# Kernel optimization log

Measured on AMD Instinct MI355X. Metric: run time of the kernel, lower is better.

## Reference

```python
import jax, jax.numpy as jnp
import numpy as np

N = 50000      # nodes
E = 800000     # edges
HID = 64       # hidden_dim
HEADS = 4
DH = HID // HEADS
PIN = 128      # person_in_dim
DIN = 64       # disease_in_dim
NEXP = 4       # num_experts
K = 2          # topk
L = 2          # n_layers
NEG = 0.2      # gat_neg_slope


def setup_inputs() -> dict:
    key = jax.random.key(0)
    ks = iter(jax.random.split(key, 64))
    nrm = lambda shp, s=0.05: jax.random.normal(next(ks), shp, jnp.float32) * s
    d = {}
    d["features"] = jax.random.normal(next(ks), (N, PIN), jnp.float32)
    d["node_types"] = jax.random.randint(next(ks), (N,), 0, 2)
    d["src"] = jax.random.randint(next(ks), (E,), 0, N)
    d["dst"] = jax.random.randint(next(ks), (E,), 0, N)
    d["W_person"] = nrm((PIN, HID)); d["b_person"] = jnp.zeros((HID,), jnp.float32)
    d["W_disease"] = nrm((DIN, HID)); d["b_disease"] = jnp.zeros((HID,), jnp.float32)
    d["gat_W"] = nrm((L, HID, HID)); d["gat_al"] = nrm((L, HEADS, DH)); d["gat_ar"] = nrm((L, HEADS, DH))
    d["gin_eps"] = jnp.zeros((L,), jnp.float32)
    d["gin_W1"] = nrm((L, HID, HID)); d["gin_b1"] = jnp.zeros((L, HID), jnp.float32)
    d["gin_W2"] = nrm((L, HID, HID)); d["gin_b2"] = jnp.zeros((L, HID), jnp.float32)
    for p in ("gat", "gin"):
        d[p + "_gW"] = nrm((HID, NEXP)); d[p + "_gb"] = jnp.zeros((NEXP,), jnp.float32)
        d[p + "_eW1"] = nrm((NEXP, HID, HID // 2)); d[p + "_eb1"] = jnp.zeros((NEXP, HID // 2), jnp.float32)
        d[p + "_eW2"] = nrm((NEXP, HID // 2, HID)); d[p + "_eb2"] = jnp.zeros((NEXP, HID), jnp.float32)
    d["fg_W1"] = nrm((2 * HID, HID)); d["fg_b1"] = jnp.zeros((HID,), jnp.float32)
    d["fg_W2"] = nrm((HID, HID)); d["fg_b2"] = jnp.zeros((HID,), jnp.float32)
    return d


def _edge_softmax(logits, dst):
    m = jax.ops.segment_max(logits, dst, num_segments=N)
    e = jnp.exp(logits - m[dst])
    s = jax.ops.segment_sum(e, dst, num_segments=N)
    return e / (s[dst] + 1e-9)


def _gat(h, src, dst, gat_W, gat_al, gat_ar):
    for l in range(L):
        hW = (h @ gat_W[l]).reshape(N, HEADS, DH)
        el = (hW * gat_al[l]).sum(-1)                    # [N, HEADS]
        er = (hW * gat_ar[l]).sum(-1)
        lg = jax.nn.leaky_relu(el[src] + er[dst], NEG)   # [E, HEADS]
        a = _edge_softmax(lg, dst)
        out = jax.ops.segment_sum(hW[src] * a[:, :, None], dst, num_segments=N)
        h2 = out.reshape(N, HID) + h                     # residual=True
        h = jax.nn.relu(h2) if l < L - 1 else h2
    return h


def _gin(h, src, dst, gin_eps, gin_W1, gin_b1, gin_W2, gin_b2):
    deg = jax.ops.segment_sum(jnp.ones((E,), jnp.float32), dst, num_segments=N)
    inv = 1.0 / jnp.maximum(deg, 1.0)
    for l in range(L):
        agg = jax.ops.segment_sum(h[src], dst, num_segments=N) * inv[:, None]  # 'mean' aggregator
        x = (1.0 + gin_eps[l]) * h + agg                 # learn_eps=True
        x = jax.nn.relu(x @ gin_W1[l] + gin_b1[l]) @ gin_W2[l] + gin_b2[l]     # 2-layer MLP
        h = jax.nn.relu(x) if l < L - 1 else x
    return h


def _expert(h, gW, gb, eW1, eb1, eW2, eb2):
    probs = jax.nn.softmax(h @ gW + gb, axis=-1)         # [N, NEXP]
    topv, topi = jax.lax.top_k(probs, K)
    topv = topv / topv.sum(-1, keepdims=True)
    hot = jax.nn.one_hot(topi, NEXP, dtype=h.dtype)      # [N, K, NEXP]
    w = (hot * topv[..., None]).sum(1)                   # [N, NEXP] sparse weights
    e1 = jax.nn.relu(jnp.einsum('nd,edh->neh', h, eW1) + eb1)
    e2 = jnp.einsum('neh,ehd->ned', e1, eW2) + eb2       # [N, NEXP, HID]
    out = (e2 * w[:, :, None]).sum(1)
    f = hot.sum(1).mean(0)                               # routed fraction per expert
    P = probs.mean(0)
    aux = NEXP * jnp.sum(f * P)                          # switch-style load balancing
    return out, aux


def reference(features, node_types, src, dst, W_person, b_person, W_disease, b_disease,
              gat_W, gat_al, gat_ar, gin_eps, gin_W1, gin_b1, gin_W2, gin_b2,
              gat_gW, gat_gb, gat_eW1, gat_eb1, gat_eW2, gat_eb2,
              gin_gW, gin_gb, gin_eW1, gin_eb1, gin_eW2, gin_eb2,
              fg_W1, fg_b1, fg_W2, fg_b2):
    # per-type projection + scatter into shared buffer
    hp = features[:, :PIN] @ W_person + b_person
    hd = features[:, :DIN] @ W_disease + b_disease
    h = jnp.where((node_types == 0)[:, None], hp, hd)
    z_gat = _gat(h, src, dst, gat_W, gat_al, gat_ar)
    z_gin = _gin(h, src, dst, gin_eps, gin_W1, gin_b1, gin_W2, gin_b2)
    zg, aux_g = _expert(z_gat, gat_gW, gat_gb, gat_eW1, gat_eb1, gat_eW2, gat_eb2)
    zi, aux_i = _expert(z_gin, gin_gW, gin_gb, gin_eW1, gin_eb1, gin_eW2, gin_eb2)
    z = zi * zg
    u = jnp.concatenate([zg, zi], axis=-1)
    gate = jax.nn.sigmoid(jax.nn.relu(u @ fg_W1 + fg_b1) @ fg_W2 + fg_b2)
    u_prime = gate  # source calls fusion_gate(u) twice -> identical deterministic value
    z = gate * z + (1.0 - gate) * u_prime
    return z, aux_i + aux_g
```

## Files before the change

### kernel.cpp

```cpp
#include <hip/hip_runtime.h>

#define NN 50000
#define EE 800000
#define NEG 0.2f
#define NBLK_SCAN 196
#define NBG 391
#define NBE 196
#define NBKT 98
#define EPB 4096
#define NSEG 196

typedef __attribute__((ext_vector_type(8))) short s8;
typedef __attribute__((ext_vector_type(4))) float f4;

__device__ __forceinline__ float leaky(float x) { return x > 0.f ? x : NEG * x; }
__device__ __forceinline__ unsigned bf16r(float x) {
    unsigned u = __float_as_uint(x);
    return (u + 0x7fffu + ((u >> 16) & 1u)) >> 16;
}
__device__ __forceinline__ float lo16(unsigned p) { return __uint_as_float(p << 16); }
__device__ __forceinline__ float hi16(unsigned p) { return __uint_as_float(p & 0xffff0000u); }

__device__ __forceinline__ s8 a_from_f32(const float* p) {
    float4 u = *reinterpret_cast<const float4*>(p);
    float4 v = *reinterpret_cast<const float4*>(p + 4);
    s8 r;
    r[0] = (short)bf16r(u.x); r[1] = (short)bf16r(u.y);
    r[2] = (short)bf16r(u.z); r[3] = (short)bf16r(u.w);
    r[4] = (short)bf16r(v.x); r[5] = (short)bf16r(v.y);
    r[6] = (short)bf16r(v.z); r[7] = (short)bf16r(v.w);
    return r;
}

__global__ __launch_bounds__(256) void k_binA(const int* __restrict__ src,
        const int* __restrict__ dst, int* __restrict__ degcnt,
        int* __restrict__ seg_off, int* __restrict__ seg_cnt,
        unsigned* __restrict__ gseg) {
    __shared__ int cnt[NBKT];
    __shared__ int pre[128];
    __shared__ unsigned sbuf[EPB];
    for (int i = threadIdx.x; i < NBKT; i += 256) cnt[i] = 0;
    __syncthreads();
    int e0 = blockIdx.x * EPB;
    int nE = EE - e0; if (nE > EPB) nE = EPB;
    int b[16]; unsigned val[16]; int rk[16];
    #pragma unroll
    for (int i = 0; i < 16; i++) {
        int li = i * 256 + threadIdx.x;
        if (li < nE) {
            int e = e0 + li;
            int d = dst[e], s = src[e];
            atomicAdd(&degcnt[d], 1);
            b[i] = d >> 9;
            val[i] = ((unsigned)s << 9) | (unsigned)(d & 511);
            rk[i] = atomicAdd(&cnt[b[i]], 1);
        } else b[i] = -1;
    }
    __syncthreads();
    if (threadIdx.x < 128) pre[threadIdx.x] = (threadIdx.x < NBKT) ? cnt[threadIdx.x] : 0;
    __syncthreads();
    for (int off = 1; off < 128; off <<= 1) {
        int v = 0;
        if (threadIdx.x < 128 && threadIdx.x >= off) v = pre[threadIdx.x - off];
        __syncthreads();
        if (threadIdx.x < 128) pre[threadIdx.x] += v;
        __syncthreads();
    }
    #pragma unroll
    for (int i = 0; i < 16; i++)
        if (b[i] >= 0) sbuf[pre[b[i]] - cnt[b[i]] + rk[i]] = val[i];
    if (threadIdx.x < NBKT) {
        seg_off[blockIdx.x * NBKT + threadIdx.x] = pre[threadIdx.x] - cnt[threadIdx.x];
        seg_cnt[blockIdx.x * NBKT + threadIdx.x] = cnt[threadIdx.x];
    }
    __syncthreads();
    for (int i = threadIdx.x; i < nE; i += 256)
        gseg[(size_t)blockIdx.x * EPB + i] = sbuf[i];
}

__global__ void k_scan_a(const int* __restrict__ degcnt, int* __restrict__ bsums) {
    __shared__ int sm[4];
    int i = blockIdx.x * 256 + threadIdx.x;
    int v = (i < NN) ? degcnt[i] : 0;
    #pragma unroll
    for (int o = 1; o < 64; o <<= 1) v += __shfl_xor(v, o, 64);
    if ((threadIdx.x & 63) == 0) sm[threadIdx.x >> 6] = v;
    __syncthreads();
    if (threadIdx.x == 0) bsums[blockIdx.x] = sm[0] + sm[1] + sm[2] + sm[3];
}

__global__ void k_scan_b(const int* __restrict__ bsums, int* __restrict__ bpre) {
    __shared__ int sm[256];
    int t = threadIdx.x;
    sm[t] = (t < NBLK_SCAN) ? bsums[t] : 0;
    __syncthreads();
    for (int off = 1; off < 256; off <<= 1) {
        int u = (t >= off) ? sm[t - off] : 0;
        __syncthreads();
        sm[t] += u;
        __syncthreads();
    }
    if (t < NBLK_SCAN) bpre[t] = (t == 0) ? 0 : sm[t - 1];
}

__global__ void k_scan_c(const int* __restrict__ degcnt, const int* __restrict__ bpre,
                         int* __restrict__ row_start) {
    __shared__ int sm[256];
    int t = threadIdx.x;
    int i = blockIdx.x * 256 + t;
    int v = (i < NN) ? degcnt[i] : 0;
    sm[t] = v;
    __syncthreads();
    for (int off = 1; off < 256; off <<= 1) {
        int u = (t >= off) ? sm[t - off] : 0;
        __syncthreads();
        sm[t] += u;
        __syncthreads();
    }
    int incl = sm[t];
    if (i < NN) row_start[i] = bpre[blockIdx.x] + incl - v;
    if (i == NN - 1) row_start[NN] = bpre[blockIdx.x] + incl;
}

__global__ __launch_bounds__(256) void k_binB_pre(
        const int* __restrict__ row_start, const int* __restrict__ seg_off,
        const int* __restrict__ seg_cnt, const unsigned* __restrict__ gseg,
        int* __restrict__ csr_src,
        const float* __restrict__ feat, const int* __restrict__ types,
        const float* __restrict__ Wp, const float* __restrict__ bp,
        const float* __restrict__ Wd, const float* __restrict__ bd,
        const float* __restrict__ gW, const float* __restrict__ al,
        const float* __restrict__ ar,
        float* __restrict__ h0f, unsigned* __restrict__ P,
        float* __restrict__ el, float* __restrict__ er) {
    __shared__ unsigned short WpT[64 * 136];
    __shared__ unsigned short WdT[64 * 72];
    __shared__ unsigned short WgT[64 * 72];
    __shared__ unsigned short y0s[4][16 * 72];
    __shared__ int kur[512];
    if (blockIdx.x < NBKT) {
        int b = blockIdx.x;
        int t = threadIdx.x;
        int* spre = (int*)WpT;
        int* soff = (int*)WdT;
        int* ss   = (int*)WgT;
        int c0 = (2 * t     < NSEG) ? seg_cnt[(2 * t)     * NBKT + b] : 0;
        int c1 = (2 * t + 1 < NSEG) ? seg_cnt[(2 * t + 1) * NBKT + b] : 0;
        if (2 * t     < NSEG) soff[2 * t]     = seg_off[(2 * t)     * NBKT + b];
        if (2 * t + 1 < NSEG) soff[2 * t + 1] = seg_off[(2 * t + 1) * NBKT + b];
        ss[t] = c0 + c1;
        __syncthreads();
        for (int off = 1; off < 256; off <<= 1) {
            int u = (t >= off) ? ss[t - off] : 0;
            __syncthreads();
            ss[t] += u;
            __syncthreads();
        }
        int base = ss[t] - (c0 + c1);
        if (2 * t     < NSEG) spre[2 * t]     = base;
        if (2 * t + 1 < NSEG) spre[2 * t + 1] = base + c0;
        if (t == 0) spre[NSEG] = ss[255];
        int d0 = b << 9;
        for (int i = t; i < 512; i += 256) {
            int d = d0 + i;
            kur[i] = (d < NN) ? row_start[d] : 0;
        }
        __syncthreads();
        int cntb = spre[NSEG];
        for (int idx = t; idx < cntb; idx += 256) {
            int lo = 0, hi = NSEG - 1;
            #pragma unroll
            for (int s = 0; s < 8; s++) {
                int mid = (lo + hi + 1) >> 1;
                if (spre[mid] <= idx) lo = mid; else hi = mid - 1;
            }
            unsigned v = gseg[(size_t)lo * EPB + soff[lo] + (idx - spre[lo])];
            int p = atomicAdd(&kur[v & 511], 1);
            csr_src[p] = (int)(v >> 9);
        }
        return;
    }
    for (int idx = threadIdx.x; idx < 128 * 64; idx += 256) {
        int k = idx >> 6, n = idx & 63;
        WpT[n * 136 + k] = (unsigned short)bf16r(Wp[idx]);
    }
    for (int idx = threadIdx.x; idx < 64 * 64; idx += 256) {
        int k = idx >> 6, n = idx & 63;
        WdT[n * 72 + k] = (unsigned short)bf16r(Wd[idx]);
        WgT[n * 72 + k] = (unsigned short)bf16r(gW[idx]);
    }
    __syncthreads();
    int wv = threadIdx.x >> 6, lane = threadIdx.x & 63;
    int quad = lane >> 4, l16 = lane & 15;
    int gw2 = (blockIdx.x - NBKT) * 4 + wv;
    int mtEnd = gw2 * 2 + 2; if (mtEnd > 3125) mtEnd = 3125;
    for (int mt = gw2 * 2; mt < mtEnd; mt++) {
        int row0 = mt * 16;
        const float* arow = feat + (size_t)(row0 + l16) * 128;
        f4 accp[4], accd[4];
        #pragma unroll
        for (int t = 0; t < 4; t++) { accp[t] = f4{0.f,0.f,0.f,0.f}; accd[t] = f4{0.f,0.f,0.f,0.f}; }
        #pragma unroll
        for (int ks = 0; ks < 4; ks++) {
            s8 a = a_from_f32(arow + ks * 32 + quad * 8);
            #pragma unroll
            for (int t = 0; t < 4; t++) {
                s8 b = *(const s8*)&WpT[(t * 16 + l16) * 136 + ks * 32 + quad * 8];
                accp[t] = __builtin_amdgcn_mfma_f32_16x16x32_bf16(a, b, accp[t], 0, 0, 0);
                if (ks < 2) {
                    s8 bd_ = *(const s8*)&WdT[(t * 16 + l16) * 72 + ks * 32 + quad * 8];
                    accd[t] = __builtin_amdgcn_mfma_f32_16x16x32_bf16(a, bd_, accd[t], 0, 0, 0);
                }
            }
        }
        int ty[4];
        #pragma unroll
        for (int r = 0; r < 4; r++) ty[r] = types[row0 + quad * 4 + r];
        float vv[4][4];
        #pragma unroll
        for (int t = 0; t < 4; t++) {
            int col = t * 16 + l16;
            float bpv = bp[col], bdv = bd[col];
            #pragma unroll
            for (int r = 0; r < 4; r++) {
                float v = ty[r] ? (accd[t][r] + bdv) : (accp[t][r] + bpv);
                vv[t][r] = v;
                h0f[(size_t)(row0 + quad * 4 + r) * 64 + col] = v;
                y0s[wv][(quad * 4 + r) * 72 + col] = (unsigned short)bf16r(v);
            }
        }
        s8 a0 = *(const s8*)&y0s[wv][l16 * 72 + quad * 8];
        s8 a1 = *(const s8*)&y0s[wv][l16 * 72 + 32 + quad * 8];
        f4 hw[4];
        #pragma unroll
        for (int t = 0; t < 4; t++) {
            hw[t] = f4{0.f,0.f,0.f,0.f};
            s8 b0 = *(const s8*)&WgT[(t * 16 + l16) * 72 + quad * 8];
            hw[t] = __builtin_amdgcn_mfma_f32_16x16x32_bf16(a0, b0, hw[t], 0, 0, 0);
            s8 b1_ = *(const s8*)&WgT[(t * 16 + l16) * 72 + 32 + quad * 8];
            hw[t] = __builtin_amdgcn_mfma_f32_16x16x32_bf16(a1, b1_, hw[t], 0, 0, 0);
        }
        #pragma unroll
        for (int t = 0; t < 4; t++) {
            int col = t * 16 + l16;
            float alv = al[col], arv = ar[col];
            #pragma unroll
            for (int r = 0; r < 4; r++) {
                int row = row0 + quad * 4 + r;
                float h = hw[t][r];
                P[(size_t)row * 64 + col] = bf16r(h) | (bf16r(vv[t][r]) << 16);
                float pl = h * alv, pr = h * arv;
                #pragma unroll
                for (int m = 1; m < 16; m <<= 1) {
                    pl += __shfl_xor(pl, m, 64);
                    pr += __shfl_xor(pr, m, 64);
                }
                if (l16 == 0) {
                    el[(size_t)row * 4 + t] = pl;
                    er[(size_t)row * 4 + t] = pr;
                }
            }
        }
    }
}

template <int RELU>
__global__ void k_edges(const int* __restrict__ rows, const int* __restrict__ csr,
                        const unsigned* __restrict__ Pin,
                        const float* __restrict__ el, const float* __restrict__ er,
                        const float* __restrict__ gat_in, const float* __restrict__ gin_in,
                        const float* __restrict__ eps_p,
                        float* __restrict__ vgf, unsigned short* __restrict__ vgb,
                        unsigned short* __restrict__ xb) {
    __shared__ float ews[4][256];
    int wv = threadIdx.x >> 6, lane = threadIdx.x & 63;
    int n = blockIdx.x * 4 + wv;
    int st = rows[n], dg = rows[n + 1] - st;
    int hd = lane >> 4;
    float4 erv = *reinterpret_cast<const float4*>(er + (size_t)n * 4);
    float accg = 0.f, acci = 0.f, ssum = 0.f;
    for (int base = 0; base < dg; base += 64) {
        int rem = dg - base; if (rem > 64) rem = 64;
        int myi = 0;
        if (lane < rem) {
            myi = csr[st + base + lane];
            float4 lv = *reinterpret_cast<const float4*>(el + (size_t)myi * 4);
            float4 ev;
            ev.x = __expf(leaky(lv.x + erv.x));
            ev.y = __expf(leaky(lv.y + erv.y));
            ev.z = __expf(leaky(lv.z + erv.z));
            ev.w = __expf(leaky(lv.w + erv.w));
            *reinterpret_cast<float4*>(&ews[wv][lane * 4]) = ev;
        }
        int j = 0;
        for (; j + 4 <= rem; j += 4) {
            int s0 = __shfl(myi, j, 64),     s1 = __shfl(myi, j + 1, 64);
            int s2 = __shfl(myi, j + 2, 64), s3 = __shfl(myi, j + 3, 64);
            unsigned p0 = Pin[(size_t)s0 * 64 + lane];
            unsigned p1 = Pin[(size_t)s1 * 64 + lane];
            unsigned p2 = Pin[(size_t)s2 * 64 + lane];
            unsigned p3 = Pin[(size_t)s3 * 64 + lane];
            float a0 = ews[wv][(j + 0) * 4 + hd];
            float a1 = ews[wv][(j + 1) * 4 + hd];
            float a2 = ews[wv][(j + 2) * 4 + hd];
            float a3 = ews[wv][(j + 3) * 4 + hd];
            accg += a0 * lo16(p0) + a1 * lo16(p1) + a2 * lo16(p2) + a3 * lo16(p3);
            acci += hi16(p0) + hi16(p1) + hi16(p2) + hi16(p3);
            ssum += a0 + a1 + a2 + a3;
        }
        for (; j < rem; j++) {
            int s0 = __shfl(myi, j, 64);
            unsigned p0 = Pin[(size_t)s0 * 64 + lane];
            float a0 = ews[wv][j * 4 + hd];
            accg += a0 * lo16(p0); acci += hi16(p0); ssum += a0;
        }
    }
    float vg = accg / (ssum + 1e-9f) + gat_in[(size_t)n * 64 + lane];
    if (RELU) vg = fmaxf(vg, 0.f);
    float invd = 1.0f / fmaxf((float)dg, 1.0f);
    float x = (1.0f + eps_p[0]) * gin_in[(size_t)n * 64 + lane] + acci * invd;
    size_t off = (size_t)n * 64 + lane;
    vgf[off] = vg;
    vgb[off] = (unsigned short)bf16r(vg);
    xb[off] = (unsigned short)bf16r(x);
}

template <int L>
__global__ __launch_bounds__(256) void k_mlp(const unsigned short* __restrict__ Gx,
        const unsigned short* __restrict__ Eb,
        const float* __restrict__ W1, const float* __restrict__ b1,
        const float* __restrict__ W2, const float* __restrict__ b2,
        const float* __restrict__ gatW, const float* __restrict__ al,
        const float* __restrict__ ar,
        unsigned short* __restrict__ Fb, float* __restrict__ Cf,
        unsigned* __restrict__ P, float* __restrict__ el, float* __restrict__ er,
        const float* __restrict__ Zg, const float* __restrict__ ggW,
        const float* __restrict__ ggb, const float* __restrict__ igW,
        const float* __restrict__ igb,
        float* __restrict__ wgtg, float* __restrict__ wgti,
        float* __restrict__ stats) {
    __shared__ unsigned short W1T[64 * 72];
    __shared__ unsigned short W2T[64 * 72];
    __shared__ unsigned short WgT[(L == 0) ? 64 * 72 : 64];
    __shared__ unsigned short y1s[4][16 * 72];
    __shared__ float sstat[16];
    if (L == 1 && threadIdx.x < 16) sstat[threadIdx.x] = 0.f;
    for (int idx = threadIdx.x; idx < 64 * 64; idx += 256) {
        int k = idx >> 6, n = idx & 63;
        W1T[n * 72 + k] = (unsigned short)bf16r(W1[idx]);
        W2T[n * 72 + k] = (unsigned short)bf16r(W2[idx]);
        if (L == 0) WgT[n * 72 + k] = (unsigned short)bf16r(gatW[idx]);
    }
    __syncthreads();
    int wv = threadIdx.x >> 6, lane = threadIdx.x & 63;
    int quad = lane >> 4, l16 = lane & 15;
    int gw = blockIdx.x * 4 + wv;
    int mtEnd = gw * 2 + 2; if (mtEnd > 3125) mtEnd = 3125;
    float sp[2][4] = {{0,0,0,0},{0,0,0,0}};
    float sh[2][4] = {{0,0,0,0},{0,0,0,0}};
    for (int mt = gw * 2; mt < mtEnd; mt++) {
        int row0 = mt * 16;
        const unsigned short* arow = Gx + (size_t)(row0 + l16) * 64;
        s8 a0 = *(const s8*)(arow + quad * 8);
        s8 a1 = *(const s8*)(arow + 32 + quad * 8);
        f4 acc1[4];
        #pragma unroll
        for (int t = 0; t < 4; t++) {
            acc1[t] = f4{0.f,0.f,0.f,0.f};
            s8 b0 = *(const s8*)&W1T[(t * 16 + l16) * 72 + quad * 8];
            acc1[t] = __builtin_amdgcn_mfma_f32_16x16x32_bf16(a0, b0, acc1[t], 0, 0, 0);
            s8 b1_ = *(const s8*)&W1T[(t * 16 + l16) * 72 + 32 + quad * 8];
            acc1[t] = __builtin_amdgcn_mfma_f32_16x16x32_bf16(a1, b1_, acc1[t], 0, 0, 0);
        }
        #pragma unroll
        for (int t = 0; t < 4; t++) {
            float b1v = b1[t * 16 + l16];
            #pragma unroll
            for (int r = 0; r < 4; r++) {
                float v = fmaxf(acc1[t][r] + b1v, 0.f);
                y1s[wv][(quad * 4 + r) * 72 + t * 16 + l16] = (unsigned short)bf16r(v);
            }
        }
        s8 c0 = *(const s8*)&y1s[wv][l16 * 72 + quad * 8];
        s8 c1 = *(const s8*)&y1s[wv][l16 * 72 + 32 + quad * 8];
        f4 acc2[4];
        #pragma unroll
        for (int t = 0; t < 4; t++) {
            acc2[t] = f4{0.f,0.f,0.f,0.f};
            s8 b0 = *(const s8*)&W2T[(t * 16 + l16) * 72 + quad * 8];
            acc2[t] = __builtin_amdgcn_mfma_f32_16x16x32_bf16(c0, b0, acc2[t], 0, 0, 0);
            s8 b1_ = *(const s8*)&W2T[(t * 16 + l16) * 72 + 32 + quad * 8];
            acc2[t] = __builtin_amdgcn_mfma_f32_16x16x32_bf16(c1, b1_, acc2[t], 0, 0, 0);
        }
        unsigned short vb[4][4];
        float vout[4][4];
        #pragma unroll
        for (int t = 0; t < 4; t++) {
            int col = t * 16 + l16;
            float b2v = b2[col];
            #pragma unroll
            for (int r = 0; r < 4; r++) {
                float v = acc2[t][r] + b2v;
                if (L == 0) v = fmaxf(v, 0.f);
                size_t off = (size_t)(row0 + quad * 4 + r) * 64 + col;
                unsigned short vb16 = (unsigned short)bf16r(v);
                vb[t][r] = vb16;
                vout[t][r] = v;
                Fb[off] = vb16;
                if (L == 0) Cf[off] = v;
            }
        }
        if (L == 0) {
            const unsigned short* erow = Eb + (size_t)(row0 + l16) * 64;
            s8 e0 = *(const s8*)(erow + quad * 8);
            s8 e1 = *(const s8*)(erow + 32 + quad * 8);
            f4 hw[4];
            #pragma unroll
            for (int t = 0; t < 4; t++) {
                hw[t] = f4{0.f,0.f,0.f,0.f};
                s8 b0 = *(const s8*)&WgT[(t * 16 + l16) * 72 + quad * 8];
                hw[t] = __builtin_amdgcn_mfma_f32_16x16x32_bf16(e0, b0, hw[t], 0, 0, 0);
                s8 b1_ = *(const s8*)&WgT[(t * 16 + l16) * 72 + 32 + quad * 8];
                hw[t] = __builtin_amdgcn_mfma_f32_16x16x32_bf16(e1, b1_, hw[t], 0, 0, 0);
            }
            #pragma unroll
            for (int t = 0; t < 4; t++) {
                int col = t * 16 + l16;
                float alv = al[col], arv = ar[col];
                #pragma unroll
                for (int r = 0; r < 4; r++) {
                    int row = row0 + quad * 4 + r;
                    float h = hw[t][r];
                    P[(size_t)row * 64 + col] = bf16r(h) | ((unsigned)vb[t][r] << 16);
                    float pl = h * alv, pr = h * arv;
                    #pragma unroll
                    for (int m = 1; m < 16; m <<= 1) {
                        pl += __shfl_xor(pl, m, 64);
                        pr += __shfl_xor(pr, m, 64);
                    }
                    if (l16 == 0) {
                        el[(size_t)row * 4 + t] = pl;
                        er[(size_t)row * 4 + t] = pr;
                    }
                }
            }
        } else {
            #pragma unroll
            for (int r = 0; r < 4; r++) {
                int row = row0 + quad * 4 + r;
                float pg[4] = {0,0,0,0}, pi[4] = {0,0,0,0};
                #pragma unroll
                for (int t = 0; t < 4; t++) {
                    int col = t * 16 + l16;
                    float zgv = Zg[(size_t)row * 64 + col];
                    float ziv = vout[t][r];
                    #pragma unroll
                    for (int e = 0; e < 4; e++) {
                        pg[e] += zgv * ggW[col * 4 + e];
                        pi[e] += ziv * igW[col * 4 + e];
                    }
                }
                #pragma unroll
                for (int m = 1; m < 16; m <<= 1) {
                    #pragma unroll
                    for (int e = 0; e < 4; e++) {
                        pg[e] += __shfl_xor(pg[e], m, 64);
                        pi[e] += __shfl_xor(pi[e], m, 64);
                    }
                }
                if (l16 == 0) {
                    #pragma unroll
                    for (int q = 0; q < 2; q++) {
                        float lg0 = (q ? pi[0] + igb[0] : pg[0] + ggb[0]);
                        float lg1 = (q ? pi[1] + igb[1] : pg[1] + ggb[1]);
                        float lg2 = (q ? pi[2] + igb[2] : pg[2] + ggb[2]);
                        float lg3 = (q ? pi[3] + igb[3] : pg[3] + ggb[3]);
                        float mx = fmaxf(fmaxf(lg0, lg1), fmaxf(lg2, lg3));
                        float ex0 = __expf(lg0 - mx), ex1 = __expf(lg1 - mx);
                        float ex2 = __expf(lg2 - mx), ex3 = __expf(lg3 - mx);
                        float inv = 1.0f / (ex0 + ex1 + ex2 + ex3);
                        float pr4[4] = {ex0 * inv, ex1 * inv, ex2 * inv, ex3 * inv};
                        int i1 = 0; float v1 = pr4[0];
                        #pragma unroll
                        for (int t = 1; t < 4; t++) if (pr4[t] > v1) { v1 = pr4[t]; i1 = t; }
                        int i2 = -1; float v2 = -1.f;
                        #pragma unroll
                        for (int t = 0; t < 4; t++) if (t != i1 && pr4[t] > v2) { v2 = pr4[t]; i2 = t; }
                        float wsum = v1 + v2;
                        float wq[4] = {0.f, 0.f, 0.f, 0.f};
                        wq[i1] = v1 / wsum; wq[i2] = v2 / wsum;
                        float* WD = q ? wgti : wgtg;
                        *reinterpret_cast<float4*>(WD + (size_t)row * 4) =
                            float4{wq[0], wq[1], wq[2], wq[3]};
                        #pragma unroll
                        for (int t = 0; t < 4; t++) sp[q][t] += pr4[t];
                        sh[q][i1] += 1.f; sh[q][i2] += 1.f;
                    }
                }
            }
        }
    }
    if (L == 1) {
        __syncthreads();
        if (l16 == 0) {
            #pragma unroll
            for (int q = 0; q < 2; q++)
                #pragma unroll
                for (int e = 0; e < 4; e++) {
                    atomicAdd(&sstat[q * 8 + e], sp[q][e]);
                    atomicAdd(&sstat[q * 8 + 4 + e], sh[q][e]);
                }
        }
        __syncthreads();
        if (threadIdx.x < 16) atomicAdd(&stats[threadIdx.x], sstat[threadIdx.x]);
    }
}

__global__ __launch_bounds__(256) void k_expert(const unsigned short* __restrict__ Eb,
        const unsigned short* __restrict__ Fb,
        const float* __restrict__ g_eW1, const float* __restrict__ g_eb1,
        const float* __restrict__ g_eW2, const float* __restrict__ g_eb2,
        const float* __restrict__ i_eW1, const float* __restrict__ i_eb1,
        const float* __restrict__ i_eW2, const float* __restrict__ i_eb2,
        const float* __restrict__ wgtg, const float* __restrict__ wgti,
        float* __restrict__ moegf, float* __restrict__ moeif,
        unsigned short* __restrict__ ub) {
    __shared__ unsigned short w1t[4 * 32 * 72];
    __shared__ unsigned short w2t[4 * 64 * 40];
    __shared__ unsigned short y1s[4][16 * 40];
    int p = (blockIdx.x >= NBE) ? 1 : 0;
    int bb = blockIdx.x - p * NBE;
    const unsigned short* Ab = p ? Fb : Eb;
    const float* eW1 = p ? i_eW1 : g_eW1;
    const float* eb1 = p ? i_eb1 : g_eb1;
    const float* eW2 = p ? i_eW2 : g_eW2;
    const float* eb2 = p ? i_eb2 : g_eb2;
    const float* wgt = p ? wgti : wgtg;
    float* moef = p ? moeif : moegf;
    int qoff = p ? 64 : 0;
    for (int g = threadIdx.x; g < 8192; g += 256) {
        int e = g >> 11, rem = g & 2047;
        int k = rem >> 5, n = rem & 31;
        w1t[e * 2304 + n * 72 + k] = (unsigned short)bf16r(eW1[g]);
    }
    for (int g = threadIdx.x; g < 8192; g += 256) {
        int e = g >> 11, rem = g & 2047;
        int k = rem >> 6, n = rem & 63;
        w2t[e * 2560 + n * 40 + k] = (unsigned short)bf16r(eW2[g]);
    }
    __syncthreads();
    int wv = threadIdx.x >> 6, lane = threadIdx.x & 63;
    int quad = lane >> 4, l16 = lane & 15;
    int gw = bb * 4 + wv;
    int mtEnd = gw * 4 + 4; if (mtEnd > 3125) mtEnd = 3125;
    for (int mt = gw * 4; mt < mtEnd; mt++) {
        int row0 = mt * 16;
        const unsigned short* arow = Ab + (size_t)(row0 + l16) * 64;
        s8 a0 = *(const s8*)(arow + quad * 8);
        s8 a1 = *(const s8*)(arow + 32 + quad * 8);
        f4 outacc[4];
        #pragma unroll
        for (int t = 0; t < 4; t++) outacc[t] = f4{0.f,0.f,0.f,0.f};
        for (int e = 0; e < 4; e++) {
            f4 acc1[2];
            #pragma unroll
            for (int t = 0; t < 2; t++) {
                acc1[t] = f4{0.f,0.f,0.f,0.f};
                s8 b0 = *(const s8*)&w1t[e * 2304 + (t * 16 + l16) * 72 + quad * 8];
                acc1[t] = __builtin_amdgcn_mfma_f32_16x16x32_bf16(a0, b0, acc1[t], 0, 0, 0);
                s8 b1_ = *(const s8*)&w1t[e * 2304 + (t * 16 + l16) * 72 + 32 + quad * 8];
                acc1[t] = __builtin_amdgcn_mfma_f32_16x16x32_bf16(a1, b1_, acc1[t], 0, 0, 0);
            }
            #pragma unroll
            for (int t = 0; t < 2; t++) {
                float b1v = eb1[e * 32 + t * 16 + l16];
                #pragma unroll
                for (int r = 0; r < 4; r++) {
                    float v = fmaxf(acc1[t][r] + b1v, 0.f);
                    y1s[wv][(quad * 4 + r) * 40 + t * 16 + l16] = (unsigned short)bf16r(v);
                }
            }
            s8 a2 = *(const s8*)&y1s[wv][l16 * 40 + quad * 8];
            f4 acc2[4];
            #pragma unroll
            for (int t = 0; t < 4; t++) {
                acc2[t] = f4{0.f,0.f,0.f,0.f};
                s8 b2_ = *(const s8*)&w2t[e * 2560 + (t * 16 + l16) * 40 + quad * 8];
                acc2[t] = __builtin_amdgcn_mfma_f32_16x16x32_bf16(a2, b2_, acc2[t], 0, 0, 0);
            }
            #pragma unroll
            for (int t = 0; t < 4; t++) {
                float b2v = eb2[e * 64 + t * 16 + l16];
                #pragma unroll
                for (int r = 0; r < 4; r++) {
                    float we = wgt[(size_t)(row0 + quad * 4 + r) * 4 + e];
                    outacc[t][r] += we * (acc2[t][r] + b2v);
                }
            }
        }
        #pragma unroll
        for (int t = 0; t < 4; t++) {
            int col = t * 16 + l16;
            #pragma unroll
            for (int r = 0; r < 4; r++) {
                int row = row0 + quad * 4 + r;
                float v = outacc[t][r];
                moef[(size_t)row * 64 + col] = v;
                ub[(size_t)row * 128 + qoff + col] = (unsigned short)bf16r(v);
            }
        }
    }
}

__global__ __launch_bounds__(256) void k_fusion(const unsigned short* __restrict__ ubuf,
        const float* __restrict__ W1, const float* __restrict__ b1,
        const float* __restrict__ W2, const float* __restrict__ b2,
        const float* __restrict__ moegf, const float* __restrict__ moeif,
        float* __restrict__ out, const float* __restrict__ stats) {
    __shared__ unsigned short W1T[64 * 136];
    __shared__ unsigned short W2T[64 * 72];
    __shared__ unsigned short y1s[4][16 * 72];
    for (int idx = threadIdx.x; idx < 128 * 64; idx += 256) {
        int k = idx >> 6, n = idx & 63;
        W1T[n * 136 + k] = (unsigned short)bf16r(W1[idx]);
    }
    for (int idx = threadIdx.x; idx < 64 * 64; idx += 256) {
        int k = idx >> 6, n = idx & 63;
        W2T[n * 72 + k] = (unsigned short)bf16r(W2[idx]);
    }
    __syncthreads();
    int wv = threadIdx.x >> 6, lane = threadIdx.x & 63;
    int quad = lane >> 4, l16 = lane & 15;
    int gw = blockIdx.x * 4 + wv;
    int mtEnd = gw * 2 + 2; if (mtEnd > 3125) mtEnd = 3125;
    for (int mt = gw * 2; mt < mtEnd; mt++) {
        int row0 = mt * 16;
        const unsigned short* arow = ubuf + (size_t)(row0 + l16) * 128;
        f4 acc1[4];
        #pragma unroll
        for (int t = 0; t < 4; t++) acc1[t] = f4{0.f,0.f,0.f,0.f};
        #pragma unroll
        for (int ks = 0; ks < 4; ks++) {
            s8 a = *(const s8*)(arow + ks * 32 + quad * 8);
            #pragma unroll
            for (int t = 0; t < 4; t++) {
                s8 b = *(const s8*)&W1T[(t * 16 + l16) * 136 + ks * 32 + quad * 8];
                acc1[t] = __builtin_amdgcn_mfma_f32_16x16x32_bf16(a, b, acc1[t], 0, 0, 0);
            }
        }
        #pragma unroll
        for (int t = 0; t < 4; t++) {
            float b1v = b1[t * 16 + l16];
            #pragma unroll
            for (int r = 0; r < 4; r++) {
                float v = fmaxf(acc1[t][r] + b1v, 0.f);
                y1s[wv][(quad * 4 + r) * 72 + t * 16 + l16] = (unsigned short)bf16r(v);
            }
        }
        f4 acc2[4];
        #pragma unroll
        for (int t = 0; t < 4; t++) acc2[t] = f4{0.f,0.f,0.f,0.f};
        #pragma unroll
        for (int ks = 0; ks < 2; ks++) {
            s8 a = *(const s8*)&y1s[wv][l16 * 72 + ks * 32 + quad * 8];
            #pragma unroll
            for (int t = 0; t < 4; t++) {
                s8 b = *(const s8*)&W2T[(t * 16 + l16) * 72 + ks * 32 + quad * 8];
                acc2[t] = __builtin_amdgcn_mfma_f32_16x16x32_bf16(a, b, acc2[t], 0, 0, 0);
            }
        }
        #pragma unroll
        for (int t = 0; t < 4; t++) {
            int col = t * 16 + l16;
            float b2v = b2[col];
            #pragma unroll
            for (int r = 0; r < 4; r++) {
                int row = row0 + quad * 4 + r;
                float g = 1.0f / (1.0f + __expf(-(acc2[t][r] + b2v)));
                float zgv = moegf[(size_t)row * 64 + col];
                float ziv = moeif[(size_t)row * 64 + col];
                out[(size_t)row * 64 + col] = g * zgv * ziv + (1.0f - g) * g;
            }
        }
    }
    if (blockIdx.x == 0 && threadIdx.x < 64) {
        int t = threadIdx.x;
        float s = (t < 16) ? stats[t] : 0.f;
        float aux = 0.f;
        for (int q = 0; q < 2; q++) {
            float a = 0.f;
            for (int e = 0; e < 4; e++) {
                float pr = __shfl(s, q * 8 + e, 64);
                float f  = __shfl(s, q * 8 + 4 + e, 64);
                a += (f / (float)NN) * (pr / (float)NN);
            }
            aux += 4.0f * a;
        }
        if (t == 0) out[(size_t)NN * 64] = aux;
    }
}

extern "C" void kernel_launch(void* const* d_in, const int* in_sizes, int n_in,
                              void* d_out, int out_size, void* d_ws, size_t ws_size,
                              hipStream_t stream) {
    (void)in_sizes; (void)n_in; (void)out_size; (void)ws_size;
    const float* features  = (const float*)d_in[0];
    const int*   node_types= (const int*)d_in[1];
    const int*   src       = (const int*)d_in[2];
    const int*   dst       = (const int*)d_in[3];
    const float* W_person  = (const float*)d_in[4];
    const float* b_person  = (const float*)d_in[5];
    const float* W_disease = (const float*)d_in[6];
    const float* b_disease = (const float*)d_in[7];
    const float* gat_W     = (const float*)d_in[8];
    const float* gat_al    = (const float*)d_in[9];
    const float* gat_ar    = (const float*)d_in[10];
    const float* gin_eps   = (const float*)d_in[11];
    const float* gin_W1    = (const float*)d_in[12];
    const float* gin_b1    = (const float*)d_in[13];
    const float* gin_W2    = (const float*)d_in[14];
    const float* gin_b2    = (const float*)d_in[15];
    const float* gat_gW    = (const float*)d_in[16];
    const float* gat_gb    = (const float*)d_in[17];
    const float* gat_eW1   = (const float*)d_in[18];
    const float* gat_eb1   = (const float*)d_in[19];
    const float* gat_eW2   = (const float*)d_in[20];
    const float* gat_eb2   = (const float*)d_in[21];
    const float* gin_gW    = (const float*)d_in[22];
    const float* gin_gb    = (const float*)d_in[23];
    const float* gin_eW1   = (const float*)d_in[24];
    const float* gin_eb1   = (const float*)d_in[25];
    const float* gin_eW2   = (const float*)d_in[26];
    const float* gin_eb2   = (const float*)d_in[27];
    const float* fg_W1     = (const float*)d_in[28];
    const float* fg_b1     = (const float*)d_in[29];
    const float* fg_W2     = (const float*)d_in[30];
    const float* fg_b2     = (const float*)d_in[31];
    float* out = (float*)d_out;

    float* ws = (float*)d_ws;
    size_t o = 0;
    float* A = ws + o; o += (size_t)NN * 64;
    float* B = ws + o; o += (size_t)NN * 64;
    float* C = ws + o; o += (size_t)NN * 64;
    unsigned short* E  = (unsigned short*)(ws + o); o += (size_t)NN * 32;
    unsigned short* F  = (unsigned short*)(ws + o); o += (size_t)NN * 32;
    unsigned short* G  = (unsigned short*)(ws + o); o += (size_t)NN * 32;
    unsigned* P = (unsigned*)(ws + o); o += (size_t)NN * 64;
    float* el = ws + o; o += (size_t)NN * 4;
    float* er = ws + o; o += (size_t)NN * 4;
    float* wgtg = ws + o; o += (size_t)NN * 4;
    float* wgti = ws + o; o += (size_t)NN * 4;
    int* degcnt    = (int*)(ws + o); o += NN;
    float* stats   = ws + o; o += 16;
    int* row_start = (int*)(ws + o); o += NN + 4;
    int* bsums     = (int*)(ws + o); o += 256;
    int* bpre      = (int*)(ws + o); o += 256;
    int* csr_src   = (int*)(ws + o); o += EE;
    int* seg_off   = (int*)(ws + o); o += NSEG * NBKT + 64;
    int* seg_cnt   = (int*)(ws + o); o += NSEG * NBKT + 64;
    unsigned* gseg = (unsigned*)(ws + o); o += (size_t)NSEG * EPB;

    unsigned short* ub = (unsigned short*)A;

    const int NB_node = NN / 4;

    hipMemsetAsync(degcnt, 0, sizeof(int) * NN + sizeof(float) * 16, stream);

    k_binA<<<NSEG, 256, 0, stream>>>(src, dst, degcnt, seg_off, seg_cnt, gseg);
    k_scan_a<<<NBLK_SCAN, 256, 0, stream>>>(degcnt, bsums);
    k_scan_b<<<1, 256, 0, stream>>>(bsums, bpre);
    k_scan_c<<<NBLK_SCAN, 256, 0, stream>>>(degcnt, bpre, row_start);

    k_binB_pre<<<NBKT + NBG, 256, 0, stream>>>(row_start, seg_off, seg_cnt, gseg, csr_src,
                                               features, node_types, W_person, b_person,
                                               W_disease, b_disease, gat_W, gat_al, gat_ar,
                                               A, P, el, er);

    k_edges<1><<<NB_node, 256, 0, stream>>>(row_start, csr_src, P, el, er, A, A,
                                            gin_eps, B, E, G);
    k_mlp<0><<<NBG, 256, 0, stream>>>(G, E, gin_W1, gin_b1, gin_W2, gin_b2,
                                      gat_W + 4096, gat_al + 64, gat_ar + 64,
                                      F, C, P, el, er,
                                      nullptr, nullptr, nullptr, nullptr, nullptr,
                                      nullptr, nullptr, nullptr);

    k_edges<0><<<NB_node, 256, 0, stream>>>(row_start, csr_src, P, el, er, B, C,
                                            gin_eps + 1, B, E, G);
    k_mlp<1><<<NBG, 256, 0, stream>>>(G, nullptr, gin_W1 + 4096, gin_b1 + 64,
                                      gin_W2 + 4096, gin_b2 + 64,
                                      nullptr, nullptr, nullptr,
                                      F, nullptr, nullptr, nullptr, nullptr,
                                      B, gat_gW, gat_gb, gin_gW, gin_gb,
                                      wgtg, wgti, stats);

    k_expert<<<NBE * 2, 256, 0, stream>>>(E, F,
                                          gat_eW1, gat_eb1, gat_eW2, gat_eb2,
                                          gin_eW1, gin_eb1, gin_eW2, gin_eb2,
                                          wgtg, wgti, B, C, ub);

    k_fusion<<<NBG, 256, 0, stream>>>(ub, fg_W1, fg_b1, fg_W2, fg_b2, B, C, out, stats);
}
```

Before: 351.5 us.

## Derive CSR row offsets inside bucket pass, drop global degree atomics and scans

Removes the per-edge global atomic degree count and the three-kernel prefix scan that built row_start. Instead, k_binA accumulates per-bucket totals, and each bucket block in k_binB_pre counts its own destination degrees in shared memory, scans them locally and writes row_start itself. This saves 800k global atomics, three launches and the large memset. The cost is that each bucket block now reads its gseg entries twice, once to count and once to scatter.

```diff
diff --git a/kernel.cpp b/kernel.cpp
--- a/kernel.cpp
+++ b/kernel.cpp
@@ -3,7 +3,6 @@
 #define NN 50000
 #define EE 800000
 #define NEG 0.2f
-#define NBLK_SCAN 196
 #define NBG 391
 #define NBE 196
 #define NBKT 98
@@ -33,9 +32,9 @@
 }
 
 __global__ __launch_bounds__(256) void k_binA(const int* __restrict__ src,
-        const int* __restrict__ dst, int* __restrict__ degcnt,
+        const int* __restrict__ dst,
         int* __restrict__ seg_off, int* __restrict__ seg_cnt,
-        unsigned* __restrict__ gseg) {
+        unsigned* __restrict__ gseg, int* __restrict__ bucket_tot) {
     __shared__ int cnt[NBKT];
     __shared__ int pre[128];
     __shared__ unsigned sbuf[EPB];
@@ -50,7 +49,6 @@
         if (li < nE) {
             int e = e0 + li;
             int d = dst[e], s = src[e];
-            atomicAdd(&degcnt[d], 1);
             b[i] = d >> 9;
             val[i] = ((unsigned)s << 9) | (unsigned)(d & 511);
             rk[i] = atomicAdd(&cnt[b[i]], 1);
@@ -72,60 +70,17 @@
     if (threadIdx.x < NBKT) {
         seg_off[blockIdx.x * NBKT + threadIdx.x] = pre[threadIdx.x] - cnt[threadIdx.x];
         seg_cnt[blockIdx.x * NBKT + threadIdx.x] = cnt[threadIdx.x];
+        atomicAdd(&bucket_tot[threadIdx.x], cnt[threadIdx.x]);
     }
     __syncthreads();
     for (int i = threadIdx.x; i < nE; i += 256)
         gseg[(size_t)blockIdx.x * EPB + i] = sbuf[i];
 }
 
-__global__ void k_scan_a(const int* __restrict__ degcnt, int* __restrict__ bsums) {
-    __shared__ int sm[4];
-    int i = blockIdx.x * 256 + threadIdx.x;
-    int v = (i < NN) ? degcnt[i] : 0;
-    #pragma unroll
-    for (int o = 1; o < 64; o <<= 1) v += __shfl_xor(v, o, 64);
-    if ((threadIdx.x & 63) == 0) sm[threadIdx.x >> 6] = v;
-    __syncthreads();
-    if (threadIdx.x == 0) bsums[blockIdx.x] = sm[0] + sm[1] + sm[2] + sm[3];
-}
-
-__global__ void k_scan_b(const int* __restrict__ bsums, int* __restrict__ bpre) {
-    __shared__ int sm[256];
-    int t = threadIdx.x;
-    sm[t] = (t < NBLK_SCAN) ? bsums[t] : 0;
-    __syncthreads();
-    for (int off = 1; off < 256; off <<= 1) {
-        int u = (t >= off) ? sm[t - off] : 0;
-        __syncthreads();
-        sm[t] += u;
-        __syncthreads();
-    }
-    if (t < NBLK_SCAN) bpre[t] = (t == 0) ? 0 : sm[t - 1];
-}
-
-__global__ void k_scan_c(const int* __restrict__ degcnt, const int* __restrict__ bpre,
-                         int* __restrict__ row_start) {
-    __shared__ int sm[256];
-    int t = threadIdx.x;
-    int i = blockIdx.x * 256 + t;
-    int v = (i < NN) ? degcnt[i] : 0;
-    sm[t] = v;
-    __syncthreads();
-    for (int off = 1; off < 256; off <<= 1) {
-        int u = (t >= off) ? sm[t - off] : 0;
-        __syncthreads();
-        sm[t] += u;
-        __syncthreads();
-    }
-    int incl = sm[t];
-    if (i < NN) row_start[i] = bpre[blockIdx.x] + incl - v;
-    if (i == NN - 1) row_start[NN] = bpre[blockIdx.x] + incl;
-}
-
 __global__ __launch_bounds__(256) void k_binB_pre(
-        const int* __restrict__ row_start, const int* __restrict__ seg_off,
+        int* __restrict__ row_start, const int* __restrict__ seg_off,
         const int* __restrict__ seg_cnt, const unsigned* __restrict__ gseg,
-        int* __restrict__ csr_src,
+        int* __restrict__ csr_src, const int* __restrict__ bucket_tot,
         const float* __restrict__ feat, const int* __restrict__ types,
         const float* __restrict__ Wp, const float* __restrict__ bp,
         const float* __restrict__ Wd, const float* __restrict__ bd,
@@ -144,12 +99,18 @@
         int* spre = (int*)WpT;
         int* soff = (int*)WdT;
         int* ss   = (int*)WgT;
+        int* sred = (int*)y0s;
+        int bt = (t < b) ? bucket_tot[t] : 0;
+        #pragma unroll
+        for (int o = 1; o < 64; o <<= 1) bt += __shfl_xor(bt, o, 64);
+        if ((t & 63) == 0) sred[t >> 6] = bt;
         int c0 = (2 * t     < NSEG) ? seg_cnt[(2 * t)     * NBKT + b] : 0;
         int c1 = (2 * t + 1 < NSEG) ? seg_cnt[(2 * t + 1) * NBKT + b] : 0;
         if (2 * t     < NSEG) soff[2 * t]     = seg_off[(2 * t)     * NBKT + b];
         if (2 * t + 1 < NSEG) soff[2 * t + 1] = seg_off[(2 * t + 1) * NBKT + b];
         ss[t] = c0 + c1;
         __syncthreads();
+        int bstart = sred[0] + sred[1] + sred[2] + sred[3];
         for (int off = 1; off < 256; off <<= 1) {
             int u = (t >= off) ? ss[t - off] : 0;
             __syncthreads();
@@ -160,13 +121,39 @@
         if (2 * t     < NSEG) spre[2 * t]     = base;
         if (2 * t + 1 < NSEG) spre[2 * t + 1] = base + c0;
         if (t == 0) spre[NSEG] = ss[255];
+        for (int i = t; i < 512; i += 256) kur[i] = 0;
+        __syncthreads();
+        int cntb = spre[NSEG];
+        for (int idx = t; idx < cntb; idx += 256) {
+            int lo = 0, hi = NSEG - 1;
+            #pragma unroll
+            for (int s = 0; s < 8; s++) {
+                int mid = (lo + hi + 1) >> 1;
+                if (spre[mid] <= idx) lo = mid; else hi = mid - 1;
+            }
+            unsigned v = gseg[(size_t)lo * EPB + soff[lo] + (idx - spre[lo])];
+            atomicAdd(&kur[v & 511], 1);
+        }
+        __syncthreads();
+        int s0 = kur[2 * t], s1 = kur[2 * t + 1];
+        int pair = s0 + s1;
+        ss[t] = pair;
+        __syncthreads();
+        for (int off = 1; off < 256; off <<= 1) {
+            int u = (t >= off) ? ss[t - off] : 0;
+            __syncthreads();
+            ss[t] += u;
+            __syncthreads();
+        }
+        int epre = ss[t] - pair;
+        int cu0 = bstart + epre, cu1 = cu0 + s0;
+        kur[2 * t] = cu0; kur[2 * t + 1] = cu1;
         int d0 = b << 9;
-        for (int i = t; i < 512; i += 256) {
-            int d = d0 + i;
-            kur[i] = (d < NN) ? row_start[d] : 0;
-        }
-        __syncthreads();
-        int cntb = spre[NSEG];
+        int d = d0 + 2 * t;
+        if (d < NN)     row_start[d]     = cu0;
+        if (d + 1 < NN) row_start[d + 1] = cu1;
+        if (b == 0 && t == 0) row_start[NN] = EE;
+        __syncthreads();
         for (int idx = t; idx < cntb; idx += 256) {
             int lo = 0, hi = NSEG - 1;
             #pragma unroll
@@ -751,11 +738,9 @@
     float* er = ws + o; o += (size_t)NN * 4;
     float* wgtg = ws + o; o += (size_t)NN * 4;
     float* wgti = ws + o; o += (size_t)NN * 4;
-    int* degcnt    = (int*)(ws + o); o += NN;
-    float* stats   = ws + o; o += 16;
+    int* bucket_tot = (int*)(ws + o); o += 112;
+    float* stats    = ws + o; o += 16;
     int* row_start = (int*)(ws + o); o += NN + 4;
-    int* bsums     = (int*)(ws + o); o += 256;
-    int* bpre      = (int*)(ws + o); o += 256;
     int* csr_src   = (int*)(ws + o); o += EE;
     int* seg_off   = (int*)(ws + o); o += NSEG * NBKT + 64;
     int* seg_cnt   = (int*)(ws + o); o += NSEG * NBKT + 64;
@@ -765,14 +750,12 @@
 
     const int NB_node = NN / 4;
 
-    hipMemsetAsync(degcnt, 0, sizeof(int) * NN + sizeof(float) * 16, stream);
-
-    k_binA<<<NSEG, 256, 0, stream>>>(src, dst, degcnt, seg_off, seg_cnt, gseg);
-    k_scan_a<<<NBLK_SCAN, 256, 0, stream>>>(degcnt, bsums);
-    k_scan_b<<<1, 256, 0, stream>>>(bsums, bpre);
-    k_scan_c<<<NBLK_SCAN, 256, 0, stream>>>(degcnt, bpre, row_start);
+    hipMemsetAsync(bucket_tot, 0, sizeof(int) * 112 + sizeof(float) * 16, stream);
+
+    k_binA<<<NSEG, 256, 0, stream>>>(src, dst, seg_off, seg_cnt, gseg, bucket_tot);
 
     k_binB_pre<<<NBKT + NBG, 256, 0, stream>>>(row_start, seg_off, seg_cnt, gseg, csr_src,
+                                               bucket_tot,
                                                features, node_types, W_person, b_person,
                                                W_disease, b_disease, gat_W, gat_al, gat_ar,
                                                A, P, el, er);
```

Measured after the change: 332.9 us. -5.3%, faster.
